# Performance work log

Hardware: AMD Instinct MI355X
Metric: run time of the kernel (lower is better)

Reference implementation:

```python
import jax, jax.numpy as jnp
import numpy as np

SCORE_THR = 0.5
IOU_THR = 0.5
N_ANCHORS = 8400  # standard YOLO 640x640 anchor count


def setup_inputs() -> dict:
    key = jax.random.key(0)
    # [1, 5, N]: channels are (cx, cy, w, h, person_conf); uniform keeps boxes/scores in [0,1)
    yolo_raw_out = jax.random.uniform(key, (1, 5, N_ANCHORS), dtype=jnp.float32)
    return {"yolo_raw_out": yolo_raw_out}


def _pairwise_iou(b):
    # b: [N,4] xyxy
    area = (b[:, 2] - b[:, 0]) * (b[:, 3] - b[:, 1])          # [N]
    lt = jnp.maximum(b[:, None, :2], b[None, :, :2])          # [N,N,2]
    rb = jnp.minimum(b[:, None, 2:], b[None, :, 2:])          # [N,N,2]
    wh = jnp.clip(rb - lt, 0.0)
    inter = wh[..., 0] * wh[..., 1]                           # [N,N]
    union = area[:, None] + area[None, :] - inter
    return inter / jnp.maximum(union, 1e-9)


def reference(yolo_raw_out):
    # permute(0,2,1).squeeze(0) -> [N,5]
    raw = yolo_raw_out[0].T
    cx, cy, w, h = raw[:, 0], raw[:, 1], raw[:, 2], raw[:, 3]
    scores = raw[:, 4]
    # cxcywh -> xyxy (torchvision.ops.box_convert)
    xyxy = jnp.stack([cx - w / 2, cy - h / 2, cx + w / 2, cy + h / 2], axis=-1)

    valid = scores >= SCORE_THR
    # sort by score descending; invalid boxes pushed to the end
    order = jnp.argsort(-jnp.where(valid, scores, -jnp.inf))
    sb = xyxy[order]          # [N,4] sorted boxes
    ss = scores[order]        # [N]
    sv = valid[order]         # [N] score-threshold mask

    iou = _pairwise_iou(sb)   # [N,N]
    n = ss.shape[0]
    idx = jnp.arange(n)

    # Greedy NMS: in score order, an active (kept, valid) box suppresses all
    # lower-scored boxes with IoU > threshold. Faithful to torchvision.ops.nms.
    def step(keep, i):
        active = keep[i]
        suppress = (iou[i] > IOU_THR) & (idx > i) & active
        return keep & ~suppress, None

    keep, _ = jax.lax.scan(step, sv, idx)

    # Fixed-shape output: kept rows carry (x1,y1,x2,y2,score); suppressed/filtered rows zeroed.
    out = jnp.concatenate([sb, ss[:, None]], axis=1) * keep[:, None].astype(ss.dtype)
    return out
```

## Files before the change

### kernel.cpp

```cpp
#include <hip/hip_runtime.h>
#include <cstdint>

#define N_ANCH 8400
#define CBLK 132
#define SCORE_THR 0.5f
#define NDIAG 8

typedef unsigned long long u64;
typedef unsigned int u32;

__device__ __forceinline__ u64 sort_key(float s, int idx) {
  u32 k32 = (s >= SCORE_THR) ? ~__float_as_uint(s) : 0xFFFFFFFFu;
  return ((u64)k32 << 32) | (u32)idx;
}

__device__ __forceinline__ u64 rfl64(u64 v) {
  u32 lo = (u32)__builtin_amdgcn_readfirstlane((int)(u32)v);
  u32 hi = (u32)__builtin_amdgcn_readfirstlane((int)(u32)(v >> 32));
  return ((u64)hi << 32) | lo;
}

__global__ void __launch_bounds__(256) rank_kernel(const float* __restrict__ raw,
                                                   float4* __restrict__ sbox,
                                                   float* __restrict__ sscore) {
  #pragma clang fp contract(off)
  int tid = blockIdx.x * 256 + threadIdx.x;
  int wid = tid >> 6, lane = tid & 63;
  int base = wid * 4;
  const float* sc = raw + 4 * N_ANCH;
  float4 sv = *(const float4*)(sc + base);
  u64 k0 = sort_key(sv.x, base),     k1 = sort_key(sv.y, base + 1);
  u64 k2 = sort_key(sv.z, base + 2), k3 = sort_key(sv.w, base + 3);
  int c0 = 0, c1 = 0, c2 = 0, c3 = 0;
  for (int it = 0; it < 33; ++it) {
    int j = it * 256 + (lane << 2);
    if (j < N_ANCH) {
      float4 q = *(const float4*)(sc + j);
      u64 a0 = sort_key(q.x, j),     a1 = sort_key(q.y, j + 1);
      u64 a2 = sort_key(q.z, j + 2), a3 = sort_key(q.w, j + 3);
      c0 += (a0 < k0) + (a1 < k0) + (a2 < k0) + (a3 < k0);
      c1 += (a0 < k1) + (a1 < k1) + (a2 < k1) + (a3 < k1);
      c2 += (a0 < k2) + (a1 < k2) + (a2 < k2) + (a3 < k2);
      c3 += (a0 < k3) + (a1 < k3) + (a2 < k3) + (a3 < k3);
    }
  }
  #pragma unroll
  for (int d = 1; d < 64; d <<= 1) {
    c0 += __shfl_xor(c0, d, 64); c1 += __shfl_xor(c1, d, 64);
    c2 += __shfl_xor(c2, d, 64); c3 += __shfl_xor(c3, d, 64);
  }
  if (lane < 4) {
    int row = base + lane;
    int cnt = (lane == 0) ? c0 : (lane == 1) ? c1 : (lane == 2) ? c2 : c3;
    float s = (lane == 0) ? sv.x : (lane == 1) ? sv.y : (lane == 2) ? sv.z : sv.w;
    float cx = raw[row], cy = raw[N_ANCH + row];
    float w = raw[2 * N_ANCH + row], h = raw[3 * N_ANCH + row];
    float hw = w * 0.5f, hh = h * 0.5f;
    sbox[cnt] = make_float4(cx - hw, cy - hh, cx + hw, cy + hh);
    sscore[cnt] = s;
  }
}

__global__ void __launch_bounds__(256) mask_kernel(const float4* __restrict__ sbox,
                                                   const float* __restrict__ sscore,
                                                   u64* __restrict__ mask,
                                                   u64* __restrict__ wlo_t) {
  #pragma clang fp contract(off)
  int cb = blockIdx.x;
  int i0 = blockIdx.y * 256;
  if (cb + 7 < (i0 >> 6)) return;
  if (!(sscore[i0] >= SCORE_THR)) return;
  if (!(sscore[cb * 64] >= SCORE_THR)) return;
  int t = threadIdx.x;
  __shared__ float4 cbox[64];
  __shared__ float carea[64];
  int j0 = cb * 64;
  if (t < 64) {
    int j = j0 + t;
    float4 bj = (j < N_ANCH) ? sbox[j] : make_float4(0.f, 0.f, 0.f, 0.f);
    cbox[t] = bj;
    carea[t] = (bj.z - bj.x) * (bj.w - bj.y);
  }
  __syncthreads();
  int i = i0 + t;
  if (i >= N_ANCH) return;
  float4 bi = sbox[i];
  float ai = (bi.z - bi.x) * (bi.w - bi.y);
  u64 wHi = 0, wLo = 0;
  for (int jj = 0; jj < 64; ++jj) {
    int jg = j0 + jj;
    float4 bb = cbox[jj];
    float ltx = fmaxf(bi.x, bb.x), lty = fmaxf(bi.y, bb.y);
    float rbx = fminf(bi.z, bb.z), rby = fminf(bi.w, bb.w);
    float wx = fmaxf(rbx - ltx, 0.f), wy = fmaxf(rby - lty, 0.f);
    float inter = wx * wy;
    float uni = (ai + carea[jj]) - inter;
    float iou = inter / fmaxf(uni, 1e-9f);
    bool sup = (iou > 0.5f) && (jg < N_ANCH);
    wHi |= (u64)(sup && (jg > i)) << jj;
    wLo |= (u64)(sup && (jg < i)) << jj;
  }
  int rb = i >> 6;
  int d = rb - cb;
  if (d < 0) {
    mask[(u64)i * CBLK + cb] = wHi;
  } else if (d < NDIAG) {
    wlo_t[((u64)d * CBLK + rb) * 64 + (i & 63)] = wLo;
  }
}

__global__ void __launch_bounds__(768, 1) nms_kernel(const float4* __restrict__ sbox,
                                                     const float* __restrict__ sscore,
                                                     const u64* __restrict__ mask,
                                                     const u64* __restrict__ wlo_t,
                                                     float* __restrict__ out) {
  __shared__ u64 keepw[CBLK + 4];
  __shared__ u64 rem[CBLK + 4];
  int tid = threadIdx.x;
  int wave = tid >> 6, lane = tid & 63;

  float s0 = sscore[lane * 132];
  u64 pb = __ballot(s0 >= SCORE_THR);
  int cnt1 = (int)__popcll(pb);
  int n_valid = 0;
  if (cnt1 > 0) {
    int a = (cnt1 - 1) * 132 + 1;
    int i1 = a + 3 * lane;
    float t1 = (i1 + 0 < N_ANCH) ? sscore[i1 + 0] : -1.f;
    float t2 = (i1 + 1 < N_ANCH) ? sscore[i1 + 1] : -1.f;
    float t3 = (i1 + 2 < N_ANCH) ? sscore[i1 + 2] : -1.f;
    u64 q1 = __ballot(t1 >= SCORE_THR);
    u64 q2 = __ballot(t2 >= SCORE_THR);
    u64 q3 = __ballot(t3 >= SCORE_THR);
    n_valid = a + (int)__popcll(q1) + (int)__popcll(q2) + (int)__popcll(q3);
  }
  int VB = (n_valid + 63) >> 6;
  int NG = (VB + 3) >> 2;

  for (int b = tid; b < CBLK + 4; b += 768) { keepw[b] = 0; rem[b] = 0; }

  int rs = (wave - 1) * 24;
  int nr = 256 - rs; if (nr > 24) nr = 24; if (nr < 0) nr = 0;

  u64 cur[26], nxt[26];
  auto wt = [&](int d, int b) -> u64 {
    return wlo_t[((u64)d * CBLK + b) * 64 + lane];
  };
  auto load_w0 = [&](int g, u64* R) {
    int b = 4 * g;
    bool k1 = (b + 1 < VB), k2 = (b + 2 < VB), k3 = (b + 3 < VB);
    R[0] = wt(0, b);
    R[1] = k1 ? wt(0, b + 1) : 0ull;
    R[2] = k2 ? wt(0, b + 2) : 0ull;
    R[3] = k3 ? wt(0, b + 3) : 0ull;
    R[4] = k1 ? wt(1, b + 1) : 0ull;
    R[5] = k2 ? wt(2, b + 2) : 0ull;
    R[6] = k2 ? wt(1, b + 2) : 0ull;
    R[7] = k3 ? wt(3, b + 3) : 0ull;
    R[8] = k3 ? wt(2, b + 3) : 0ull;
    R[9] = k3 ? wt(1, b + 3) : 0ull;
    #pragma unroll
    for (int m = 0; m < 4; ++m) {
      int c = b + 4 + m;
      bool ok = (c < VB);
      #pragma unroll
      for (int j = 0; j < 4; ++j)
        R[10 + m * 4 + j] = ok ? wt(4 + m - j, c) : 0ull;
    }
  };
  auto fixpoint = [&](u64 colw, u64 act) -> u64 {
    u64 U = act, K = 0;
    while (U) {
      u64 covered = __ballot((colw & U) != 0ull);
      u64 dead    = __ballot((colw & K) != 0ull);
      u64 nk = U & ~covered & ~dead;
      K |= nk;
      U &= ~(nk | dead);
    }
    return K;
  };

  u64 P0 = 0, P1 = 0, P2 = 0, P3 = 0;

  if (wave == 0 && NG > 0) load_w0(0, cur);

  for (int g = 0; g < NG; ++g) {
    asm volatile("s_waitcnt lgkmcnt(0)\ns_barrier" ::: "memory");

    if (wave == 0) {
      __builtin_amdgcn_s_setprio(1);
      int b = 4 * g;
      u64 r0 = rem[b], r1 = rem[b + 1], r2 = rem[b + 2], r3 = rem[b + 3];
      if (g > 0) {
        #pragma unroll
        for (int i = 0; i < 26; ++i) cur[i] = nxt[i];
      }
      if (g + 1 < NG) load_w0(g + 1, nxt);

      int remn = n_valid - b * 64;
      u64 vm0, vm1, vm2, vm3;
      {
        int m0 = remn, m1 = remn - 64, m2 = remn - 128, m3 = remn - 192;
        vm0 = (m0 >= 64) ? ~0ull : ((m0 <= 0) ? 0ull : ((1ull << m0) - 1ull));
        vm1 = (m1 >= 64) ? ~0ull : ((m1 <= 0) ? 0ull : ((1ull << m1) - 1ull));
        vm2 = (m2 >= 64) ? ~0ull : ((m2 <= 0) ? 0ull : ((1ull << m2) - 1ull));
        vm3 = (m3 >= 64) ? ~0ull : ((m3 <= 0) ? 0ull : ((1ull << m3) - 1ull));
      }
      u64 act0 = vm0 & ~(rfl64(r0) | P0);
      u64 act1 = vm1 & ~(rfl64(r1) | P1);
      u64 act2 = vm2 & ~(rfl64(r2) | P2);
      u64 act3 = vm3 & ~(rfl64(r3) | P3);

      u64 kw0 = fixpoint(cur[0], act0);
      u64 s1 = __ballot((cur[4] & kw0) != 0ull);
      u64 kw1 = fixpoint(cur[1], act1 & ~s1);
      u64 s2 = __ballot(((cur[5] & kw0) | (cur[6] & kw1)) != 0ull);
      u64 kw2 = fixpoint(cur[2], act2 & ~s2);
      u64 s3 = __ballot(((cur[7] & kw0) | (cur[8] & kw1) | (cur[9] & kw2)) != 0ull);
      u64 kw3 = fixpoint(cur[3], act3 & ~s3);

      if (lane == 0) {
        keepw[b] = kw0; keepw[b + 1] = kw1;
        keepw[b + 2] = kw2; keepw[b + 3] = kw3;
      }

      P0 = __ballot(((cur[10] & kw0) | (cur[11] & kw1) |
                     (cur[12] & kw2) | (cur[13] & kw3)) != 0ull);
      P1 = __ballot(((cur[14] & kw0) | (cur[15] & kw1) |
                     (cur[16] & kw2) | (cur[17] & kw3)) != 0ull);
      P2 = __ballot(((cur[18] & kw0) | (cur[19] & kw1) |
                     (cur[20] & kw2) | (cur[21] & kw3)) != 0ull);
      P3 = __ballot(((cur[22] & kw0) | (cur[23] & kw1) |
                     (cur[24] & kw2) | (cur[25] & kw3)) != 0ull);
      __builtin_amdgcn_s_setprio(0);
    } else if (g >= 1 && nr > 0) {
      int e = g - 1;
      int base = 4 * e + 8;
      if (base < VB) {
        int wi = rs >> 6, sh = rs & 63;
        u64 lo = keepw[4 * e + wi];
        u64 hi = (sh + nr > 64 && wi < 3) ? keepw[4 * e + wi + 1] : 0ull;
        u64 window = sh ? ((lo >> sh) | (hi << (64 - sh))) : lo;
        window = rfl64(window);
        const u64* pr = mask + (u64)(256 * e + rs) * CBLK;
        int cL = base + lane;
        bool okL = (cL < VB);
        u64 acc = 0;
        #pragma unroll
        for (int r = 0; r < 24; ++r) {
          bool bit = (r < nr) && (((window >> r) & 1ull) != 0ull);
          u64 v = (bit && okL) ? pr[(u64)r * CBLK + cL] : 0ull;
          acc |= v;
        }
        if (okL && acc) atomicOr((unsigned long long*)&rem[cL], acc);
        if (base + 64 < VB) {
          int cH = cL + 64;
          bool okH = (cH < VB);
          u64 acc2 = 0;
          #pragma unroll
          for (int r = 0; r < 24; ++r) {
            bool bit = (r < nr) && (((window >> r) & 1ull) != 0ull);
            u64 v = (bit && okH) ? pr[(u64)r * CBLK + cH] : 0ull;
            acc2 |= v;
          }
          if (okH && acc2) atomicOr((unsigned long long*)&rem[cH], acc2);
        }
      }
    }
  }
  __syncthreads();

  for (int r2 = tid; r2 < N_ANCH; r2 += 768) {
    u64 kv = keepw[r2 >> 6];
    bool kp = (kv >> (r2 & 63)) & 1ull;
    float4 b4 = sbox[r2];
    float sc = sscore[r2];
    float* o = out + r2 * 5;
    o[0] = kp ? b4.x : 0.f;
    o[1] = kp ? b4.y : 0.f;
    o[2] = kp ? b4.z : 0.f;
    o[3] = kp ? b4.w : 0.f;
    o[4] = kp ? sc : 0.f;
  }
}

extern "C" void kernel_launch(void* const* d_in, const int* in_sizes, int n_in,
                              void* d_out, int out_size, void* d_ws, size_t ws_size,
                              hipStream_t stream) {
  const float* raw = (const float*)d_in[0];
  float* out = (float*)d_out;
  char* ws = (char*)d_ws;
  float4* sbox = (float4*)ws;
  float* sscore = (float*)(ws + 8448 * 16);
  u64* mask = (u64*)(ws + 8448 * 16 + 8448 * 4);
  u64* wlo_t = (u64*)(ws + 8448 * 16 + 8448 * 4 + (size_t)N_ANCH * CBLK * 8);

  rank_kernel<<<525, 256, 0, stream>>>(raw, sbox, sscore);
  mask_kernel<<<dim3(CBLK, 33), 256, 0, stream>>>(sbox, sscore, mask, wlo_t);
  nms_kernel<<<1, 768, 0, stream>>>(sbox, sscore, mask, wlo_t, out);
}
```

Measured before the change: 130.5 us.

## Deepen NMS pipeline: widen diagonal band and split helper loads from reductions

Widens the locally resolved diagonal band from 8 to 12 column blocks, so wave 0 propagates suppression two groups ahead and helper waves get an extra group of slack. Helper waves now issue their mask-row loads into registers one group before reducing and OR-ing them into the shared remove list. This hides global load latency behind the serial fixpoint loop. The block shrinks from 768 to 512 threads, with 37 rows per helper wave. Register pressure rises (42+42 carried words, 74 staging words), and mask_kernel writes more diagonal data.

Result: slower. 171.7 us (+31.5%).

```diff
diff --git a/kernel.cpp b/kernel.cpp
--- a/kernel.cpp
+++ b/kernel.cpp
@@ -4,7 +4,7 @@
 #define N_ANCH 8400
 #define CBLK 132
 #define SCORE_THR 0.5f
-#define NDIAG 8
+#define NDIAG 12
 
 typedef unsigned long long u64;
 typedef unsigned int u32;
@@ -68,7 +68,7 @@
   #pragma clang fp contract(off)
   int cb = blockIdx.x;
   int i0 = blockIdx.y * 256;
-  if (cb + 7 < (i0 >> 6)) return;
+  if (cb + 11 < (i0 >> 6)) return;
   if (!(sscore[i0] >= SCORE_THR)) return;
   if (!(sscore[cb * 64] >= SCORE_THR)) return;
   int t = threadIdx.x;
@@ -109,7 +109,7 @@
   }
 }
 
-__global__ void __launch_bounds__(768, 1) nms_kernel(const float4* __restrict__ sbox,
+__global__ void __launch_bounds__(512, 1) nms_kernel(const float4* __restrict__ sbox,
                                                      const float* __restrict__ sscore,
                                                      const u64* __restrict__ mask,
                                                      const u64* __restrict__ wlo_t,
@@ -137,12 +137,13 @@
   int VB = (n_valid + 63) >> 6;
   int NG = (VB + 3) >> 2;
 
-  for (int b = tid; b < CBLK + 4; b += 768) { keepw[b] = 0; rem[b] = 0; }
-
-  int rs = (wave - 1) * 24;
-  int nr = 256 - rs; if (nr > 24) nr = 24; if (nr < 0) nr = 0;
-
-  u64 cur[26], nxt[26];
+  for (int b = tid; b < CBLK + 4; b += 512) { keepw[b] = 0; rem[b] = 0; }
+
+  int rs = (wave - 1) * 37;
+  int nr = 256 - rs; if (nr > 37) nr = 37; if (nr < 0) nr = 0;
+  u64 tl[37], th[37];
+
+  u64 cur[42], nxt[42];
   auto wt = [&](int d, int b) -> u64 {
     return wlo_t[((u64)d * CBLK + b) * 64 + lane];
   };
@@ -160,7 +161,7 @@
     R[8] = k3 ? wt(2, b + 3) : 0ull;
     R[9] = k3 ? wt(1, b + 3) : 0ull;
     #pragma unroll
-    for (int m = 0; m < 4; ++m) {
+    for (int m = 0; m < 8; ++m) {
       int c = b + 4 + m;
       bool ok = (c < VB);
       #pragma unroll
@@ -180,7 +181,8 @@
     return K;
   };
 
-  u64 P0 = 0, P1 = 0, P2 = 0, P3 = 0;
+  u64 land0 = 0, land1 = 0, land2 = 0, land3 = 0;
+  u64 c20 = 0, c21 = 0, c22 = 0, c23 = 0;
 
   if (wave == 0 && NG > 0) load_w0(0, cur);
 
@@ -193,7 +195,7 @@
       u64 r0 = rem[b], r1 = rem[b + 1], r2 = rem[b + 2], r3 = rem[b + 3];
       if (g > 0) {
         #pragma unroll
-        for (int i = 0; i < 26; ++i) cur[i] = nxt[i];
+        for (int i = 0; i < 42; ++i) cur[i] = nxt[i];
       }
       if (g + 1 < NG) load_w0(g + 1, nxt);
 
@@ -206,10 +208,10 @@
         vm2 = (m2 >= 64) ? ~0ull : ((m2 <= 0) ? 0ull : ((1ull << m2) - 1ull));
         vm3 = (m3 >= 64) ? ~0ull : ((m3 <= 0) ? 0ull : ((1ull << m3) - 1ull));
       }
-      u64 act0 = vm0 & ~(rfl64(r0) | P0);
-      u64 act1 = vm1 & ~(rfl64(r1) | P1);
-      u64 act2 = vm2 & ~(rfl64(r2) | P2);
-      u64 act3 = vm3 & ~(rfl64(r3) | P3);
+      u64 act0 = vm0 & ~(rfl64(r0) | land0);
+      u64 act1 = vm1 & ~(rfl64(r1) | land1);
+      u64 act2 = vm2 & ~(rfl64(r2) | land2);
+      u64 act3 = vm3 & ~(rfl64(r3) | land3);
 
       u64 kw0 = fixpoint(cur[0], act0);
       u64 s1 = __ballot((cur[4] & kw0) != 0ull);
@@ -224,53 +226,70 @@
         keepw[b + 2] = kw2; keepw[b + 3] = kw3;
       }
 
-      P0 = __ballot(((cur[10] & kw0) | (cur[11] & kw1) |
-                     (cur[12] & kw2) | (cur[13] & kw3)) != 0ull);
-      P1 = __ballot(((cur[14] & kw0) | (cur[15] & kw1) |
-                     (cur[16] & kw2) | (cur[17] & kw3)) != 0ull);
-      P2 = __ballot(((cur[18] & kw0) | (cur[19] & kw1) |
-                     (cur[20] & kw2) | (cur[21] & kw3)) != 0ull);
-      P3 = __ballot(((cur[22] & kw0) | (cur[23] & kw1) |
-                     (cur[24] & kw2) | (cur[25] & kw3)) != 0ull);
+      u64 F[8];
+      #pragma unroll
+      for (int m = 0; m < 8; ++m) {
+        F[m] = __ballot(((cur[10 + 4 * m + 0] & kw0) |
+                         (cur[10 + 4 * m + 1] & kw1) |
+                         (cur[10 + 4 * m + 2] & kw2) |
+                         (cur[10 + 4 * m + 3] & kw3)) != 0ull);
+      }
+      land0 = F[0] | c20; land1 = F[1] | c21;
+      land2 = F[2] | c22; land3 = F[3] | c23;
+      c20 = F[4]; c21 = F[5]; c22 = F[6]; c23 = F[7];
       __builtin_amdgcn_s_setprio(0);
-    } else if (g >= 1 && nr > 0) {
-      int e = g - 1;
-      int base = 4 * e + 8;
-      if (base < VB) {
-        int wi = rs >> 6, sh = rs & 63;
-        u64 lo = keepw[4 * e + wi];
-        u64 hi = (sh + nr > 64 && wi < 3) ? keepw[4 * e + wi + 1] : 0ull;
-        u64 window = sh ? ((lo >> sh) | (hi << (64 - sh))) : lo;
-        window = rfl64(window);
-        const u64* pr = mask + (u64)(256 * e + rs) * CBLK;
-        int cL = base + lane;
-        bool okL = (cL < VB);
-        u64 acc = 0;
-        #pragma unroll
-        for (int r = 0; r < 24; ++r) {
-          bool bit = (r < nr) && (((window >> r) & 1ull) != 0ull);
-          u64 v = (bit && okL) ? pr[(u64)r * CBLK + cL] : 0ull;
-          acc |= v;
+    } else if (nr > 0) {
+      if (g >= 2) {
+        int e = g - 2;
+        int base = 4 * e + 12;
+        if (base < VB) {
+          u64 acc = 0;
+          #pragma unroll
+          for (int r = 0; r < 37; ++r) acc |= tl[r];
+          int cL = base + lane;
+          if (cL < VB && acc) atomicOr((unsigned long long*)&rem[cL], acc);
+          if (base + 64 < VB) {
+            u64 acc2 = 0;
+            #pragma unroll
+            for (int r = 0; r < 37; ++r) acc2 |= th[r];
+            int cH = cL + 64;
+            if (cH < VB && acc2) atomicOr((unsigned long long*)&rem[cH], acc2);
+          }
         }
-        if (okL && acc) atomicOr((unsigned long long*)&rem[cL], acc);
-        if (base + 64 < VB) {
-          int cH = cL + 64;
-          bool okH = (cH < VB);
-          u64 acc2 = 0;
+      }
+      if (g >= 1) {
+        int e = g - 1;
+        int base = 4 * e + 12;
+        if (base < VB) {
+          int wi = rs >> 6, sh = rs & 63;
+          u64 lo = keepw[4 * e + wi];
+          u64 hi = (sh + nr > 64 && wi < 3) ? keepw[4 * e + wi + 1] : 0ull;
+          u64 window = sh ? ((lo >> sh) | (hi << (64 - sh))) : lo;
+          window = rfl64(window);
+          const u64* pr = mask + (u64)(256 * e + rs) * CBLK;
+          int cL = base + lane;
+          bool okL = (cL < VB);
           #pragma unroll
-          for (int r = 0; r < 24; ++r) {
+          for (int r = 0; r < 37; ++r) {
             bool bit = (r < nr) && (((window >> r) & 1ull) != 0ull);
-            u64 v = (bit && okH) ? pr[(u64)r * CBLK + cH] : 0ull;
-            acc2 |= v;
+            tl[r] = (bit && okL) ? pr[(u64)r * CBLK + cL] : 0ull;
           }
-          if (okH && acc2) atomicOr((unsigned long long*)&rem[cH], acc2);
+          if (base + 64 < VB) {
+            int cH = cL + 64;
+            bool okH = (cH < VB);
+            #pragma unroll
+            for (int r = 0; r < 37; ++r) {
+              bool bit = (r < nr) && (((window >> r) & 1ull) != 0ull);
+              th[r] = (bit && okH) ? pr[(u64)r * CBLK + cH] : 0ull;
+            }
+          }
         }
       }
     }
   }
   __syncthreads();
 
-  for (int r2 = tid; r2 < N_ANCH; r2 += 768) {
+  for (int r2 = tid; r2 < N_ANCH; r2 += 512) {
     u64 kv = keepw[r2 >> 6];
     bool kp = (kv >> (r2 & 63)) & 1ull;
     float4 b4 = sbox[r2];
@@ -297,5 +316,5 @@
 
   rank_kernel<<<525, 256, 0, stream>>>(raw, sbox, sscore);
   mask_kernel<<<dim3(CBLK, 33), 256, 0, stream>>>(sbox, sscore, mask, wlo_t);
-  nms_kernel<<<1, 768, 0, stream>>>(sbox, sscore, mask, wlo_t, out);
-}
+  nms_kernel<<<1, 512, 0, stream>>>(sbox, sscore, mask, wlo_t, out);
+}
```

## Prefetch next group's suppression mask rows into registers; skip useless IoU tiles early

Applied to the files above, without the earlier changes.

In the NMS kernel, helper waves now load the mask rows for the next group into a register array while the leader wave resolves the current group. When keep bits arrive, the low-column accumulation uses register masking instead of dependent global loads, which takes memory latency off the serial chain. The mask kernel now exits early for tiles beyond the diagonal band and builds a single bitword rather than two. This costs 24 more registers per helper lane and adds speculative loads of rows that may never be needed.

Measured after the change: 307.5 us. 136% more time.

```diff
diff --git a/kernel.cpp b/kernel.cpp
--- a/kernel.cpp
+++ b/kernel.cpp
@@ -84,9 +84,13 @@
   __syncthreads();
   int i = i0 + t;
   if (i >= N_ANCH) return;
+  int rb = i >> 6;
+  int d = rb - cb;
+  if (d >= NDIAG) return;
+  bool hi = (d < 0);
   float4 bi = sbox[i];
   float ai = (bi.z - bi.x) * (bi.w - bi.y);
-  u64 wHi = 0, wLo = 0;
+  u64 w = 0;
   for (int jj = 0; jj < 64; ++jj) {
     int jg = j0 + jj;
     float4 bb = cbox[jj];
@@ -97,15 +101,13 @@
     float uni = (ai + carea[jj]) - inter;
     float iou = inter / fmaxf(uni, 1e-9f);
     bool sup = (iou > 0.5f) && (jg < N_ANCH);
-    wHi |= (u64)(sup && (jg > i)) << jj;
-    wLo |= (u64)(sup && (jg < i)) << jj;
-  }
-  int rb = i >> 6;
-  int d = rb - cb;
-  if (d < 0) {
-    mask[(u64)i * CBLK + cb] = wHi;
-  } else if (d < NDIAG) {
-    wlo_t[((u64)d * CBLK + rb) * 64 + (i & 63)] = wLo;
+    bool cond = hi ? (jg > i) : (jg < i);
+    w |= (u64)(sup && cond) << jj;
+  }
+  if (hi) {
+    mask[(u64)i * CBLK + cb] = w;
+  } else {
+    wlo_t[((u64)d * CBLK + rb) * 64 + (i & 63)] = w;
   }
 }
 
@@ -141,6 +143,7 @@
 
   int rs = (wave - 1) * 24;
   int nr = 256 - rs; if (nr > 24) nr = 24; if (nr < 0) nr = 0;
+  u64 tl[24];
 
   u64 cur[26], nxt[26];
   auto wt = [&](int d, int b) -> u64 {
@@ -233,37 +236,52 @@
       P3 = __ballot(((cur[22] & kw0) | (cur[23] & kw1) |
                      (cur[24] & kw2) | (cur[25] & kw3)) != 0ull);
       __builtin_amdgcn_s_setprio(0);
-    } else if (g >= 1 && nr > 0) {
-      int e = g - 1;
-      int base = 4 * e + 8;
-      if (base < VB) {
-        int wi = rs >> 6, sh = rs & 63;
-        u64 lo = keepw[4 * e + wi];
-        u64 hi = (sh + nr > 64 && wi < 3) ? keepw[4 * e + wi + 1] : 0ull;
-        u64 window = sh ? ((lo >> sh) | (hi << (64 - sh))) : lo;
-        window = rfl64(window);
-        const u64* pr = mask + (u64)(256 * e + rs) * CBLK;
-        int cL = base + lane;
-        bool okL = (cL < VB);
-        u64 acc = 0;
-        #pragma unroll
-        for (int r = 0; r < 24; ++r) {
-          bool bit = (r < nr) && (((window >> r) & 1ull) != 0ull);
-          u64 v = (bit && okL) ? pr[(u64)r * CBLK + cL] : 0ull;
-          acc |= v;
-        }
-        if (okL && acc) atomicOr((unsigned long long*)&rem[cL], acc);
-        if (base + 64 < VB) {
-          int cH = cL + 64;
-          bool okH = (cH < VB);
-          u64 acc2 = 0;
+    } else if (nr > 0) {
+      if (g >= 1) {
+        int e = g - 1;
+        int base = 4 * e + 8;
+        if (base < VB) {
+          int wi = rs >> 6, sh = rs & 63;
+          u64 lo = keepw[4 * e + wi];
+          u64 hi = (sh + nr > 64 && wi < 3) ? keepw[4 * e + wi + 1] : 0ull;
+          u64 window = sh ? ((lo >> sh) | (hi << (64 - sh))) : lo;
+          window = rfl64(window);
+          int cL = base + lane;
+          bool okL = (cL < VB);
+          u64 acc = 0;
           #pragma unroll
           for (int r = 0; r < 24; ++r) {
-            bool bit = (r < nr) && (((window >> r) & 1ull) != 0ull);
-            u64 v = (bit && okH) ? pr[(u64)r * CBLK + cH] : 0ull;
-            acc2 |= v;
+            u64 sm = (u64)0 - ((window >> r) & 1ull);
+            acc |= tl[r] & sm;
           }
-          if (okH && acc2) atomicOr((unsigned long long*)&rem[cH], acc2);
+          if (okL && acc) atomicOr((unsigned long long*)&rem[cL], acc);
+          if (base + 64 < VB) {
+            int cH = cL + 64;
+            bool okH = (cH < VB);
+            const u64* pr = mask + (u64)(256 * e + rs) * CBLK;
+            u64 acc2 = 0;
+            #pragma unroll
+            for (int r = 0; r < 24; ++r) {
+              bool bit = (r < nr) && (((window >> r) & 1ull) != 0ull);
+              bool rok = (256 * e + rs + r) < N_ANCH;
+              u64 v = (bit && okH && rok) ? pr[(u64)r * CBLK + cH] : 0ull;
+              acc2 |= v;
+            }
+            if (okH && acc2) atomicOr((unsigned long long*)&rem[cH], acc2);
+          }
+        }
+      }
+      {
+        int base2 = 4 * g + 8;
+        if (base2 < VB) {
+          const u64* pr2 = mask + (u64)(256 * g + rs) * CBLK;
+          int cL2 = base2 + lane;
+          bool ok2 = (cL2 < VB);
+          #pragma unroll
+          for (int r = 0; r < 24; ++r) {
+            bool rok = (r < nr) && ((256 * g + rs + r) < N_ANCH);
+            tl[r] = (ok2 && rok) ? pr2[(u64)r * CBLK + cL2] : 0ull;
+          }
         }
       }
     }
```
